# Performance work log

Measured on AMD Instinct MI355X. Metric: run time of the kernel, lower is better.

The kernel has to match this reference:

```python
import jax, jax.numpy as jnp
import numpy as np
from jax import lax


def _viterbi_decode(logits, trans):
    """Batched Viterbi decode (tf.contrib.crf.crf_decode semantics, full lengths).
    logits: [B, T, U] unary potentials; trans: [U, U], trans[i, j] = score(i -> j).
    Returns int32 tags [B, T]."""
    logits_t = jnp.swapaxes(logits, 0, 1)  # [T, B, U]
    init_v = logits_t[0]                   # [B, U]

    def fwd_step(v, logit_t):
        # scores[b, i, j] = v[b, i] + trans[i, j]
        scores = v[:, :, None] + trans[None, :, :]          # [B, U, U]
        bp = jnp.argmax(scores, axis=1).astype(jnp.int32)   # [B, U] best prev tag
        v_new = jnp.max(scores, axis=1) + logit_t           # [B, U]
        return v_new, bp

    v_last, bps = lax.scan(fwd_step, init_v, logits_t[1:])  # bps: [T-1, B, U]
    last_tag = jnp.argmax(v_last, axis=1).astype(jnp.int32)  # [B]

    def bwd_step(tag, bp):
        # tag is the tag at t+1; bp[b, k] = best tag at t given tag k at t+1
        new_tag = jnp.take_along_axis(bp, tag[:, None], axis=1)[:, 0]
        return new_tag, new_tag

    _, tags_prefix = lax.scan(bwd_step, last_tag, bps, reverse=True)  # [T-1, B]
    tags = jnp.concatenate([tags_prefix, last_tag[None, :]], axis=0)  # [T, B]
    return jnp.swapaxes(tags, 0, 1)  # [B, T]


def setup_inputs() -> dict:
    key = jax.random.key(0)
    k0, k1, k2, k3, k4 = jax.random.split(key, 5)
    B, T, D, U = 64, 512, 1024, 128
    x = jax.random.normal(k0, (B, T, D), dtype=jnp.float32)
    kernel = jax.random.normal(k1, (D, U), dtype=jnp.float32) * (1.0 / np.sqrt(D))
    bias = jnp.zeros((U,), dtype=jnp.float32)
    chain_kernel = jax.random.normal(k2, (U, U), dtype=jnp.float32) * 0.1
    left_boundary = jax.random.normal(k3, (U,), dtype=jnp.float32) * 0.1
    right_boundary = jax.random.normal(k4, (U,), dtype=jnp.float32) * 0.1
    return {
        "x": x,
        "kernel": kernel,
        "bias": bias,
        "chain_kernel": chain_kernel,
        "left_boundary": left_boundary,
        "right_boundary": right_boundary,
    }


def reference(x, kernel, bias, chain_kernel, left_boundary, right_boundary):
    # _dense_layer: linear activation, x @ kernel + bias
    logits = jnp.einsum("btd,du->btu", x, kernel) + bias  # [B, T, U]
    # add_boundary_energy with mask=None: boundaries on first / last timestep
    logits = logits.at[:, 0, :].add(left_boundary)
    logits = logits.at[:, -1, :].add(right_boundary)
    # test_mode='viterbi', learn_mode='join': return decoded tags cast to float32
    tags = _viterbi_decode(logits, chain_kernel)
    return tags.astype(jnp.float32)
```

## Files before the change

kernel.cpp:

```cpp
#include <hip/hip_runtime.h>

#define T_SEQ 512
#define U_TAGS 128
#define D_DIM 1024
#define M_ROWS (64 * T_SEQ)

__global__ __launch_bounds__(256, 4) void crf_gemm_part(
    const float* __restrict__ A, const float* __restrict__ Bk,
    float* __restrict__ Cpart, int kdepth) {
  __shared__ float As[16][132];
  __shared__ float Bs[16][132];
  const int tid = threadIdx.x;
  const int tx = tid & 15, ty = tid >> 4;
  const int row0 = blockIdx.x * 128;
  const int kbase = blockIdx.y * kdepth;

  const int am = tid >> 2, ak = (tid & 3) << 2;
  const int bk = tid >> 5, bn = (tid & 31) << 2;

  float acc[8][8] = {};

  float4 a0 = *(const float4*)&A[(size_t)(row0 + am) * D_DIM + kbase + ak];
  float4 a1 = *(const float4*)&A[(size_t)(row0 + am + 64) * D_DIM + kbase + ak];
  float4 b0 = *(const float4*)&Bk[(size_t)(kbase + bk) * U_TAGS + bn];
  float4 b1 = *(const float4*)&Bk[(size_t)(kbase + bk + 8) * U_TAGS + bn];

  for (int k0 = 0; k0 < kdepth; k0 += 16) {
    As[ak + 0][am] = a0.x; As[ak + 1][am] = a0.y;
    As[ak + 2][am] = a0.z; As[ak + 3][am] = a0.w;
    As[ak + 0][am + 64] = a1.x; As[ak + 1][am + 64] = a1.y;
    As[ak + 2][am + 64] = a1.z; As[ak + 3][am + 64] = a1.w;
    *(float4*)&Bs[bk][bn] = b0;
    *(float4*)&Bs[bk + 8][bn] = b1;
    __syncthreads();
    if (k0 + 16 < kdepth) {
      const int kn = kbase + k0 + 16;
      a0 = *(const float4*)&A[(size_t)(row0 + am) * D_DIM + kn + ak];
      a1 = *(const float4*)&A[(size_t)(row0 + am + 64) * D_DIM + kn + ak];
      b0 = *(const float4*)&Bk[(size_t)(kn + bk) * U_TAGS + bn];
      b1 = *(const float4*)&Bk[(size_t)(kn + bk + 8) * U_TAGS + bn];
    }
#pragma unroll
    for (int kk = 0; kk < 16; ++kk) {
      float a[8], b[8];
      *(float4*)&a[0] = *(const float4*)&As[kk][ty * 8];
      *(float4*)&a[4] = *(const float4*)&As[kk][ty * 8 + 4];
      *(float4*)&b[0] = *(const float4*)&Bs[kk][tx * 4];
      *(float4*)&b[4] = *(const float4*)&Bs[kk][tx * 4 + 64];
#pragma unroll
      for (int r = 0; r < 8; ++r)
#pragma unroll
        for (int c = 0; c < 8; ++c) acc[r][c] = fmaf(a[r], b[c], acc[r][c]);
    }
    __syncthreads();
  }

  float* Cp = Cpart + (size_t)blockIdx.y * M_ROWS * U_TAGS;
#pragma unroll
  for (int r = 0; r < 8; ++r) {
    const int row = row0 + ty * 8 + r;
    *(float4*)&Cp[(size_t)row * U_TAGS + tx * 4] = *(float4*)&acc[r][0];
    *(float4*)&Cp[(size_t)row * U_TAGS + tx * 4 + 64] = *(float4*)&acc[r][4];
  }
}

__global__ __launch_bounds__(256) void crf_combine(
    float* __restrict__ p, const float* __restrict__ bias,
    const float* __restrict__ lb, const float* __restrict__ rb, int nparts) {
  const int i = blockIdx.x * 256 + threadIdx.x;
  const int row = i >> 5;
  const int col = (i & 31) << 2;
  const int t = row & (T_SEQ - 1);
  float4 o = *(const float4*)&p[(size_t)i * 4];
  for (int q = 1; q < nparts; ++q) {
    const float* pq = p + (size_t)q * M_ROWS * U_TAGS;
    float4 v = *(const float4*)&pq[(size_t)i * 4];
    o.x += v.x; o.y += v.y; o.z += v.z; o.w += v.w;
  }
  float4 bb = *(const float4*)&bias[col];
  o.x += bb.x; o.y += bb.y; o.z += bb.z; o.w += bb.w;
  if (t == 0) {
    float4 l = *(const float4*)&lb[col];
    o.x += l.x; o.y += l.y; o.z += l.z; o.w += l.w;
  }
  if (t == T_SEQ - 1) {
    float4 r = *(const float4*)&rb[col];
    o.x += r.x; o.y += r.y; o.z += r.z; o.w += r.w;
  }
  *(float4*)&p[(size_t)i * 4] = o;
}

__global__ __launch_bounds__(256) void crf_gemm(
    const float* __restrict__ A, const float* __restrict__ Bk,
    const float* __restrict__ bias, const float* __restrict__ lb,
    const float* __restrict__ rb, float* __restrict__ C) {
  __shared__ float As[16][132];
  __shared__ float Bs[16][132];
  const int tid = threadIdx.x;
  const int tx = tid & 15, ty = tid >> 4;
  const int row0 = blockIdx.x * 128;
  const int am = tid >> 2, ak = (tid & 3) << 2;
  const int bk = tid >> 5, bn = (tid & 31) << 2;
  float acc[8][8] = {};
  float4 a0 = *(const float4*)&A[(size_t)(row0 + am) * D_DIM + ak];
  float4 a1 = *(const float4*)&A[(size_t)(row0 + am + 64) * D_DIM + ak];
  float4 b0 = *(const float4*)&Bk[(size_t)bk * U_TAGS + bn];
  float4 b1 = *(const float4*)&Bk[(size_t)(bk + 8) * U_TAGS + bn];
  for (int k0 = 0; k0 < D_DIM; k0 += 16) {
    As[ak + 0][am] = a0.x; As[ak + 1][am] = a0.y;
    As[ak + 2][am] = a0.z; As[ak + 3][am] = a0.w;
    As[ak + 0][am + 64] = a1.x; As[ak + 1][am + 64] = a1.y;
    As[ak + 2][am + 64] = a1.z; As[ak + 3][am + 64] = a1.w;
    *(float4*)&Bs[bk][bn] = b0;
    *(float4*)&Bs[bk + 8][bn] = b1;
    __syncthreads();
    if (k0 + 16 < D_DIM) {
      a0 = *(const float4*)&A[(size_t)(row0 + am) * D_DIM + k0 + 16 + ak];
      a1 = *(const float4*)&A[(size_t)(row0 + am + 64) * D_DIM + k0 + 16 + ak];
      b0 = *(const float4*)&Bk[(size_t)(k0 + 16 + bk) * U_TAGS + bn];
      b1 = *(const float4*)&Bk[(size_t)(k0 + 16 + bk + 8) * U_TAGS + bn];
    }
#pragma unroll
    for (int kk = 0; kk < 16; ++kk) {
      float a[8], b[8];
      *(float4*)&a[0] = *(const float4*)&As[kk][ty * 8];
      *(float4*)&a[4] = *(const float4*)&As[kk][ty * 8 + 4];
      *(float4*)&b[0] = *(const float4*)&Bs[kk][tx * 4];
      *(float4*)&b[4] = *(const float4*)&Bs[kk][tx * 4 + 64];
#pragma unroll
      for (int r = 0; r < 8; ++r)
#pragma unroll
        for (int c = 0; c < 8; ++c) acc[r][c] = fmaf(a[r], b[c], acc[r][c]);
    }
    __syncthreads();
  }
#pragma unroll
  for (int r = 0; r < 8; ++r) {
    const int row = row0 + ty * 8 + r;
    const int t = row & (T_SEQ - 1);
    const int n0 = tx * 4, n1 = tx * 4 + 64;
    float o[8];
#pragma unroll
    for (int c = 0; c < 4; ++c) {
      float v = acc[r][c] + bias[n0 + c];
      if (t == 0) v += lb[n0 + c];
      if (t == T_SEQ - 1) v += rb[n0 + c];
      o[c] = v;
    }
#pragma unroll
    for (int c = 0; c < 4; ++c) {
      float v = acc[r][c + 4] + bias[n1 + c];
      if (t == 0) v += lb[n1 + c];
      if (t == T_SEQ - 1) v += rb[n1 + c];
      o[c + 4] = v;
    }
    *(float4*)&C[(size_t)row * U_TAGS + n0] = *(float4*)&o[0];
    *(float4*)&C[(size_t)row * U_TAGS + n1] = *(float4*)&o[4];
  }
}

__device__ __forceinline__ float rl_f(float v, int lane) {
  return __int_as_float(__builtin_amdgcn_readlane(__float_as_int(v), lane));
}
template <int CTRL>
__device__ __forceinline__ float dpp_max_step(float x) {
  int v = __float_as_int(x);
  int t = __builtin_amdgcn_update_dpp(v, v, CTRL, 0xF, 0xF, false);
  return fmaxf(x, __int_as_float(t));
}
__device__ __forceinline__ float wave_max64_bcast(float x) {
  x = dpp_max_step<0x111>(x);
  x = dpp_max_step<0x112>(x);
  x = dpp_max_step<0x114>(x);
  x = dpp_max_step<0x118>(x);
  x = dpp_max_step<0x142>(x);
  x = dpp_max_step<0x143>(x);
  return rl_f(x, 63);
}

__global__ __launch_bounds__(256) void crf_viterbi(
    const float* __restrict__ logits,
    const float* __restrict__ trans,
    float* __restrict__ out) {
  __shared__ __align__(16) float trs[U_TAGS * U_TAGS];
  __shared__ __align__(16) unsigned char bp[(T_SEQ - 1) * U_TAGS];
  __shared__ unsigned char tags[T_SEQ];
  __shared__ unsigned char M[8][U_TAGS];
  __shared__ float rmaxs[U_TAGS];
  __shared__ float wmin2[2];
  __shared__ float gminS;
  __shared__ int lastTagS;

  const int b = blockIdx.x;
  const int tid = threadIdx.x;
  const float* lg_b = logits + (size_t)b * T_SEQ * U_TAGS;

#pragma unroll
  for (int it = 0; it < 16; ++it)
    *(float4*)&trs[(it * 256 + tid) * 4] =
        *(const float4*)&trans[(it * 256 + tid) * 4];
  __syncthreads();

  float rowmin = 1e30f;
  if (tid < U_TAGS) {
    float mx = -1e30f, mn = 1e30f;
    for (int q = 0; q < 32; ++q) {
      float4 v = *(const float4*)&trs[tid * U_TAGS + q * 4];
      mx = fmaxf(fmaxf(mx, v.x), fmaxf(v.y, fmaxf(v.z, v.w)));
      mn = fminf(fminf(mn, v.x), fminf(v.y, fminf(v.z, v.w)));
    }
    rmaxs[tid] = mx;
    rowmin = mn;
  }
  if (tid < U_TAGS) {
#pragma unroll
    for (int off = 1; off < 64; off <<= 1)
      rowmin = fminf(rowmin, __shfl_xor(rowmin, off));
    if ((tid & 63) == 0) wmin2[tid >> 6] = rowmin;
  }
  __syncthreads();
  if (tid == 0) gminS = fminf(wmin2[0], wmin2[1]);
  __syncthreads();

  if (tid < 64) {
    const int l = tid;
    float v0 = lg_b[l];
    float v1 = lg_b[64 + l];
    const float gmin = gminS;
    const float c0 = rmaxs[l] - gmin + 0.01f;
    const float c1 = rmaxs[64 + l] - gmin + 0.01f;
    float lgA0 = lg_b[U_TAGS + l], lgA1 = lg_b[U_TAGS + 64 + l];
    float lgB0 = lg_b[2 * U_TAGS + l], lgB1 = lg_b[2 * U_TAGS + 64 + l];

    for (int t = 1; t < T_SEQ; ++t) {
      int tp = t + 2; if (tp > T_SEQ - 1) tp = T_SEQ - 1;
      float lgC0 = lg_b[(size_t)tp * U_TAGS + l];
      float lgC1 = lg_b[(size_t)tp * U_TAGS + 64 + l];

      const float vm = wave_max64_bcast(fmaxf(v0, v1));
      unsigned long long m0 = __ballot(v0 + c0 >= vm);
      unsigned long long m1 = __ballot(v1 + c1 >= vm);

      int a0 = -1, a1 = -1, b0 = -1, b1 = -1;
      if (m0) { a0 = __builtin_ctzll(m0); m0 &= m0 - 1;
        if (m0) { a1 = __builtin_ctzll(m0); m0 &= m0 - 1; } }
      if (m1) { b0 = __builtin_ctzll(m1); m1 &= m1 - 1;
        if (m1) { b1 = __builtin_ctzll(m1); m1 &= m1 - 1; } }

      float tA00 = 0, tA01 = 0, tA10 = 0, tA11 = 0;
      float tB00 = 0, tB01 = 0, tB10 = 0, tB11 = 0;
      if (a0 >= 0) { tA00 = trs[a0 * U_TAGS + l]; tA01 = trs[a0 * U_TAGS + 64 + l]; }
      if (a1 >= 0) { tA10 = trs[a1 * U_TAGS + l]; tA11 = trs[a1 * U_TAGS + 64 + l]; }
      if (b0 >= 0) { tB00 = trs[(64 + b0) * U_TAGS + l]; tB01 = trs[(64 + b0) * U_TAGS + 64 + l]; }
      if (b1 >= 0) { tB10 = trs[(64 + b1) * U_TAGS + l]; tB11 = trs[(64 + b1) * U_TAGS + 64 + l]; }

      float best0 = -1e30f, best1 = -1e30f;
      int bi0 = 0, bi1 = 0;
      if (a0 >= 0) {
        float vi = rl_f(v0, a0);
        float s0 = vi + tA00, s1 = vi + tA01;
        if (s0 > best0) { best0 = s0; bi0 = a0; }
        if (s1 > best1) { best1 = s1; bi1 = a0; }
      }
      if (a1 >= 0) {
        float vi = rl_f(v0, a1);
        float s0 = vi + tA10, s1 = vi + tA11;
        if (s0 > best0) { best0 = s0; bi0 = a1; }
        if (s1 > best1) { best1 = s1; bi1 = a1; }
      }
      while (m0) {
        int i = __builtin_ctzll(m0); m0 &= m0 - 1;
        float vi = rl_f(v0, i);
        float s0 = vi + trs[i * U_TAGS + l], s1 = vi + trs[i * U_TAGS + 64 + l];
        if (s0 > best0) { best0 = s0; bi0 = i; }
        if (s1 > best1) { best1 = s1; bi1 = i; }
      }
      if (b0 >= 0) {
        float vi = rl_f(v1, b0);
        float s0 = vi + tB00, s1 = vi + tB01;
        if (s0 > best0) { best0 = s0; bi0 = 64 + b0; }
        if (s1 > best1) { best1 = s1; bi1 = 64 + b0; }
      }
      if (b1 >= 0) {
        float vi = rl_f(v1, b1);
        float s0 = vi + tB10, s1 = vi + tB11;
        if (s0 > best0) { best0 = s0; bi0 = 64 + b1; }
        if (s1 > best1) { best1 = s1; bi1 = 64 + b1; }
      }
      while (m1) {
        int i = __builtin_ctzll(m1); m1 &= m1 - 1;
        float vi = rl_f(v1, i);
        float s0 = vi + trs[(64 + i) * U_TAGS + l];
        float s1 = vi + trs[(64 + i) * U_TAGS + 64 + l];
        if (s0 > best0) { best0 = s0; bi0 = 64 + i; }
        if (s1 > best1) { best1 = s1; bi1 = 64 + i; }
      }

      bp[(t - 1) * U_TAGS + l] = (unsigned char)bi0;
      bp[(t - 1) * U_TAGS + 64 + l] = (unsigned char)bi1;
      v0 = best0 + lgA0;
      v1 = best1 + lgA1;
      lgA0 = lgB0; lgA1 = lgB1;
      lgB0 = lgC0; lgB1 = lgC1;
    }

    float val = v0; int idx = l;
    if (v1 > v0) { val = v1; idx = 64 + l; }
#pragma unroll
    for (int off = 1; off < 64; off <<= 1) {
      float vo = __shfl_xor(val, off);
      int io = __shfl_xor(idx, off);
      if (vo > val || (vo == val && io < idx)) { val = vo; idx = io; }
    }
    if (l == 0) { lastTagS = idx; tags[T_SEQ - 1] = (unsigned char)idx; }
  }
  __syncthreads();

#pragma unroll
  for (int q = 0; q < 4; ++q) {
    const int chain = tid + q * 256;
    const int c = chain >> 7, s = chain & 127;
    const int lo = c * 64;
    const int hi = (c == 7) ? (T_SEQ - 2) : (c * 64 + 63);
    int cur = s;
    for (int t = hi; t >= lo; --t) cur = bp[t * U_TAGS + cur];
    M[c][s] = (unsigned char)cur;
  }
  __syncthreads();
  __shared__ unsigned char seedE[8];
  if (tid == 0) {
    int e = lastTagS;
    seedE[7] = (unsigned char)e;
    for (int c = 7; c >= 1; --c) { e = M[c][e]; seedE[c - 1] = (unsigned char)e; }
  }
  __syncthreads();
  if (tid < 8) {
    const int c = tid;
    const int lo = c * 64;
    const int hi = (c == 7) ? (T_SEQ - 2) : (c * 64 + 63);
    int cur = seedE[c];
    for (int t = hi; t >= lo; --t) {
      cur = bp[t * U_TAGS + cur];
      tags[t] = (unsigned char)cur;
    }
  }
  __syncthreads();
  out[(size_t)b * T_SEQ + tid] = (float)tags[tid];
  out[(size_t)b * T_SEQ + 256 + tid] = (float)tags[256 + tid];
}

extern "C" void kernel_launch(void* const* d_in, const int* in_sizes, int n_in,
                              void* d_out, int out_size, void* d_ws,
                              size_t ws_size, hipStream_t stream) {
  const float* x = (const float*)d_in[0];
  const float* kern = (const float*)d_in[1];
  const float* bias = (const float*)d_in[2];
  const float* chain = (const float*)d_in[3];
  const float* lb = (const float*)d_in[4];
  const float* rb = (const float*)d_in[5];
  float* out = (float*)d_out;
  float* logits = (float*)d_ws;

  const size_t part = (size_t)M_ROWS * U_TAGS * sizeof(float);
  const int nblk = M_ROWS * U_TAGS / 4 / 256;
  if (ws_size >= 4 * part) {
    crf_gemm_part<<<dim3(256, 4), 256, 0, stream>>>(x, kern, logits, D_DIM / 4);
    crf_combine<<<nblk, 256, 0, stream>>>(logits, bias, lb, rb, 4);
  } else if (ws_size >= 2 * part) {
    crf_gemm_part<<<dim3(256, 2), 256, 0, stream>>>(x, kern, logits, D_DIM / 2);
    crf_combine<<<nblk, 256, 0, stream>>>(logits, bias, lb, rb, 2);
  } else {
    crf_gemm<<<256, 256, 0, stream>>>(x, kern, bias, lb, rb, logits);
  }
  crf_viterbi<<<64, 256, 0, stream>>>(logits, chain, out);
}
```

Baseline: 671.7 us.

## Shrink GEMM tiles to 64 rows and branchlessly unroll Viterbi candidate max

The split-K GEMM now uses 64-row tiles with 128-thread blocks, doubling the block count so more CUs receive work. The Viterbi step handles the first four candidate predecessors per half with branch-free readlanes, LDS loads and a tournament of selects, and falls back to a loop only when more candidates remain. This shortens the serial per-timestep critical path, which dominates since only 64 blocks run. The cost is lower register reuse in the GEMM and extra work when few candidates exist, and tie-breaking between candidates changes.

```diff
diff --git a/kernel.cpp b/kernel.cpp
--- a/kernel.cpp
+++ b/kernel.cpp
@@ -5,40 +5,46 @@
 #define D_DIM 1024
 #define M_ROWS (64 * T_SEQ)
 
-__global__ __launch_bounds__(256, 4) void crf_gemm_part(
+__global__ __launch_bounds__(128) void crf_gemm_part(
     const float* __restrict__ A, const float* __restrict__ Bk,
     float* __restrict__ Cpart, int kdepth) {
-  __shared__ float As[16][132];
+  __shared__ float As[16][68];
   __shared__ float Bs[16][132];
   const int tid = threadIdx.x;
   const int tx = tid & 15, ty = tid >> 4;
-  const int row0 = blockIdx.x * 128;
+  const int row0 = blockIdx.x * 64;
   const int kbase = blockIdx.y * kdepth;
 
-  const int am = tid >> 2, ak = (tid & 3) << 2;
-  const int bk = tid >> 5, bn = (tid & 31) << 2;
+  const int am = tid >> 1, ak = (tid & 1) << 3;
+  const int bk0 = tid >> 5, bn = (tid & 31) << 2;
 
   float acc[8][8] = {};
 
   float4 a0 = *(const float4*)&A[(size_t)(row0 + am) * D_DIM + kbase + ak];
-  float4 a1 = *(const float4*)&A[(size_t)(row0 + am + 64) * D_DIM + kbase + ak];
-  float4 b0 = *(const float4*)&Bk[(size_t)(kbase + bk) * U_TAGS + bn];
-  float4 b1 = *(const float4*)&Bk[(size_t)(kbase + bk + 8) * U_TAGS + bn];
+  float4 a1 = *(const float4*)&A[(size_t)(row0 + am) * D_DIM + kbase + ak + 4];
+  float4 b0 = *(const float4*)&Bk[(size_t)(kbase + bk0) * U_TAGS + bn];
+  float4 b1 = *(const float4*)&Bk[(size_t)(kbase + bk0 + 4) * U_TAGS + bn];
+  float4 b2 = *(const float4*)&Bk[(size_t)(kbase + bk0 + 8) * U_TAGS + bn];
+  float4 b3 = *(const float4*)&Bk[(size_t)(kbase + bk0 + 12) * U_TAGS + bn];
 
   for (int k0 = 0; k0 < kdepth; k0 += 16) {
     As[ak + 0][am] = a0.x; As[ak + 1][am] = a0.y;
     As[ak + 2][am] = a0.z; As[ak + 3][am] = a0.w;
-    As[ak + 0][am + 64] = a1.x; As[ak + 1][am + 64] = a1.y;
-    As[ak + 2][am + 64] = a1.z; As[ak + 3][am + 64] = a1.w;
-    *(float4*)&Bs[bk][bn] = b0;
-    *(float4*)&Bs[bk + 8][bn] = b1;
+    As[ak + 4][am] = a1.x; As[ak + 5][am] = a1.y;
+    As[ak + 6][am] = a1.z; As[ak + 7][am] = a1.w;
+    *(float4*)&Bs[bk0][bn] = b0;
+    *(float4*)&Bs[bk0 + 4][bn] = b1;
+    *(float4*)&Bs[bk0 + 8][bn] = b2;
+    *(float4*)&Bs[bk0 + 12][bn] = b3;
     __syncthreads();
     if (k0 + 16 < kdepth) {
       const int kn = kbase + k0 + 16;
       a0 = *(const float4*)&A[(size_t)(row0 + am) * D_DIM + kn + ak];
-      a1 = *(const float4*)&A[(size_t)(row0 + am + 64) * D_DIM + kn + ak];
-      b0 = *(const float4*)&Bk[(size_t)(kn + bk) * U_TAGS + bn];
-      b1 = *(const float4*)&Bk[(size_t)(kn + bk + 8) * U_TAGS + bn];
+      a1 = *(const float4*)&A[(size_t)(row0 + am) * D_DIM + kn + ak + 4];
+      b0 = *(const float4*)&Bk[(size_t)(kn + bk0) * U_TAGS + bn];
+      b1 = *(const float4*)&Bk[(size_t)(kn + bk0 + 4) * U_TAGS + bn];
+      b2 = *(const float4*)&Bk[(size_t)(kn + bk0 + 8) * U_TAGS + bn];
+      b3 = *(const float4*)&Bk[(size_t)(kn + bk0 + 12) * U_TAGS + bn];
     }
 #pragma unroll
     for (int kk = 0; kk < 16; ++kk) {
@@ -177,6 +183,12 @@
   x = dpp_max_step<0x143>(x);
   return rl_f(x, 63);
 }
+__device__ __forceinline__ void win(float sa, int ia, float sb, int ib,
+                                    float& so, int& io) {
+  bool g = sa >= sb;
+  so = g ? sa : sb;
+  io = g ? ia : ib;
+}
 
 __global__ __launch_bounds__(256) void crf_viterbi(
     const float* __restrict__ logits,
@@ -241,65 +253,78 @@
       unsigned long long m0 = __ballot(v0 + c0 >= vm);
       unsigned long long m1 = __ballot(v1 + c1 >= vm);
 
-      int a0 = -1, a1 = -1, b0 = -1, b1 = -1;
-      if (m0) { a0 = __builtin_ctzll(m0); m0 &= m0 - 1;
-        if (m0) { a1 = __builtin_ctzll(m0); m0 &= m0 - 1; } }
-      if (m1) { b0 = __builtin_ctzll(m1); m1 &= m1 - 1;
-        if (m1) { b1 = __builtin_ctzll(m1); m1 &= m1 - 1; } }
-
-      float tA00 = 0, tA01 = 0, tA10 = 0, tA11 = 0;
-      float tB00 = 0, tB01 = 0, tB10 = 0, tB11 = 0;
-      if (a0 >= 0) { tA00 = trs[a0 * U_TAGS + l]; tA01 = trs[a0 * U_TAGS + 64 + l]; }
-      if (a1 >= 0) { tA10 = trs[a1 * U_TAGS + l]; tA11 = trs[a1 * U_TAGS + 64 + l]; }
-      if (b0 >= 0) { tB00 = trs[(64 + b0) * U_TAGS + l]; tB01 = trs[(64 + b0) * U_TAGS + 64 + l]; }
-      if (b1 >= 0) { tB10 = trs[(64 + b1) * U_TAGS + l]; tB11 = trs[(64 + b1) * U_TAGS + 64 + l]; }
-
-      float best0 = -1e30f, best1 = -1e30f;
-      int bi0 = 0, bi1 = 0;
-      if (a0 >= 0) {
-        float vi = rl_f(v0, a0);
-        float s0 = vi + tA00, s1 = vi + tA01;
-        if (s0 > best0) { best0 = s0; bi0 = a0; }
-        if (s1 > best1) { best1 = s1; bi1 = a0; }
+      unsigned long long r0 = m0, r1 = m1;
+      int i0[4], i1[4];
+      bool f0[4], f1[4];
+#pragma unroll
+      for (int s = 0; s < 4; ++s) {
+        f0[s] = (r0 != 0ull);
+        i0[s] = __builtin_ctzll(r0 | 0x8000000000000000ull);
+        r0 &= r0 - 1;
+        f1[s] = (r1 != 0ull);
+        i1[s] = __builtin_ctzll(r1 | 0x8000000000000000ull);
+        r1 &= r1 - 1;
       }
-      if (a1 >= 0) {
-        float vi = rl_f(v0, a1);
-        float s0 = vi + tA10, s1 = vi + tA11;
-        if (s0 > best0) { best0 = s0; bi0 = a1; }
-        if (s1 > best1) { best1 = s1; bi1 = a1; }
+      float sv0[4], sv1[4];
+#pragma unroll
+      for (int s = 0; s < 4; ++s) {
+        sv0[s] = f0[s] ? rl_f(v0, i0[s]) : -1e30f;
+        sv1[s] = f1[s] ? rl_f(v1, i1[s]) : -1e30f;
       }
-      while (m0) {
-        int i = __builtin_ctzll(m0); m0 &= m0 - 1;
-        float vi = rl_f(v0, i);
-        float s0 = vi + trs[i * U_TAGS + l], s1 = vi + trs[i * U_TAGS + 64 + l];
-        if (s0 > best0) { best0 = s0; bi0 = i; }
-        if (s1 > best1) { best1 = s1; bi1 = i; }
+      float tA[4][2], tB[4][2];
+#pragma unroll
+      for (int s = 0; s < 4; ++s) {
+        const float* pA = &trs[i0[s] * U_TAGS + l];
+        tA[s][0] = pA[0]; tA[s][1] = pA[64];
+        const float* pB = &trs[(64 + i1[s]) * U_TAGS + l];
+        tB[s][0] = pB[0]; tB[s][1] = pB[64];
       }
-      if (b0 >= 0) {
-        float vi = rl_f(v1, b0);
-        float s0 = vi + tB00, s1 = vi + tB01;
-        if (s0 > best0) { best0 = s0; bi0 = 64 + b0; }
-        if (s1 > best1) { best1 = s1; bi1 = 64 + b0; }
+      float sAL[4], sAH[4], sBL[4], sBH[4];
+#pragma unroll
+      for (int s = 0; s < 4; ++s) {
+        sAL[s] = sv0[s] + tA[s][0]; sAH[s] = sv0[s] + tA[s][1];
+        sBL[s] = sv1[s] + tB[s][0]; sBH[s] = sv1[s] + tB[s][1];
       }
-      if (b1 >= 0) {
-        float vi = rl_f(v1, b1);
-        float s0 = vi + tB10, s1 = vi + tB11;
-        if (s0 > best0) { best0 = s0; bi0 = 64 + b1; }
-        if (s1 > best1) { best1 = s1; bi1 = 64 + b1; }
+      float wL, wL2, wL3, wL4, wH, wH2, wH3, wH4;
+      int xL, xL2, xL3, xL4, xH, xH2, xH3, xH4;
+      win(sAL[0], i0[0], sAL[1], i0[1], wL, xL);
+      win(sAL[2], i0[2], sAL[3], i0[3], wL2, xL2);
+      win(sBL[0], 64 + i1[0], sBL[1], 64 + i1[1], wL3, xL3);
+      win(sBL[2], 64 + i1[2], sBL[3], 64 + i1[3], wL4, xL4);
+      win(wL, xL, wL2, xL2, wL, xL);
+      win(wL3, xL3, wL4, xL4, wL3, xL3);
+      win(wL, xL, wL3, xL3, wL, xL);
+      win(sAH[0], i0[0], sAH[1], i0[1], wH, xH);
+      win(sAH[2], i0[2], sAH[3], i0[3], wH2, xH2);
+      win(sBH[0], 64 + i1[0], sBH[1], 64 + i1[1], wH3, xH3);
+      win(sBH[2], 64 + i1[2], sBH[3], 64 + i1[3], wH4, xH4);
+      win(wH, xH, wH2, xH2, wH, xH);
+      win(wH3, xH3, wH4, xH4, wH3, xH3);
+      win(wH, xH, wH3, xH3, wH, xH);
+
+      if (r0 | r1) {
+        while (r0) {
+          int i = __builtin_ctzll(r0); r0 &= r0 - 1;
+          float vi = rl_f(v0, i);
+          float sL = vi + trs[i * U_TAGS + l];
+          float sH = vi + trs[i * U_TAGS + 64 + l];
+          if (sL > wL || (sL == wL && i < xL)) { wL = sL; xL = i; }
+          if (sH > wH || (sH == wH && i < xH)) { wH = sH; xH = i; }
+        }
+        while (r1) {
+          int i = __builtin_ctzll(r1); r1 &= r1 - 1;
+          float vi = rl_f(v1, i);
+          float sL = vi + trs[(64 + i) * U_TAGS + l];
+          float sH = vi + trs[(64 + i) * U_TAGS + 64 + l];
+          if (sL > wL || (sL == wL && 64 + i < xL)) { wL = sL; xL = 64 + i; }
+          if (sH > wH || (sH == wH && 64 + i < xH)) { wH = sH; xH = 64 + i; }
+        }
       }
-      while (m1) {
-        int i = __builtin_ctzll(m1); m1 &= m1 - 1;
-        float vi = rl_f(v1, i);
-        float s0 = vi + trs[(64 + i) * U_TAGS + l];
-        float s1 = vi + trs[(64 + i) * U_TAGS + 64 + l];
-        if (s0 > best0) { best0 = s0; bi0 = 64 + i; }
-        if (s1 > best1) { best1 = s1; bi1 = 64 + i; }
-      }
-
-      bp[(t - 1) * U_TAGS + l] = (unsigned char)bi0;
-      bp[(t - 1) * U_TAGS + 64 + l] = (unsigned char)bi1;
-      v0 = best0 + lgA0;
-      v1 = best1 + lgA1;
+
+      bp[(t - 1) * U_TAGS + l] = (unsigned char)xL;
+      bp[(t - 1) * U_TAGS + 64 + l] = (unsigned char)xH;
+      v0 = wL + lgA0;
+      v1 = wH + lgA1;
       lgA0 = lgB0; lgA1 = lgB1;
       lgB0 = lgC0; lgB1 = lgC1;
     }
@@ -364,10 +389,10 @@
   const size_t part = (size_t)M_ROWS * U_TAGS * sizeof(float);
   const int nblk = M_ROWS * U_TAGS / 4 / 256;
   if (ws_size >= 4 * part) {
-    crf_gemm_part<<<dim3(256, 4), 256, 0, stream>>>(x, kern, logits, D_DIM / 4);
+    crf_gemm_part<<<dim3(512, 4), 128, 0, stream>>>(x, kern, logits, D_DIM / 4);
     crf_combine<<<nblk, 256, 0, stream>>>(logits, bias, lb, rb, 4);
   } else if (ws_size >= 2 * part) {
-    crf_gemm_part<<<dim3(256, 2), 256, 0, stream>>>(x, kern, logits, D_DIM / 2);
+    crf_gemm_part<<<dim3(512, 2), 128, 0, stream>>>(x, kern, logits, D_DIM / 2);
     crf_combine<<<nblk, 256, 0, stream>>>(logits, bias, lb, rb, 2);
   } else {
     crf_gemm<<<256, 256, 0, stream>>>(x, kern, bias, lb, rb, logits);
```

Result: no change. 668.0 us (-0.5%).

## Add producer-wave logit prefetch ring and branchless top-3 Viterbi selection; use 2-way split-K

Applied to the files above, without the earlier changes.

The Viterbi kernel now dedicates a second wavefront to streaming each sequence's logits from global memory into a 4-slot shared-memory ring buffer, synchronised through volatile flags. The compute wave reads each step's logits from LDS instead of issuing global loads inside the serial recurrence. The candidate-predecessor search is also rebuilt as an unconditional top-3-per-half selection with select-based comparisons, falling back to a loop only when there are more candidates. Separately, the GEMM drops the 4-way split-K path for a fixed 2-way split, which halves the combine kernel's partial-sum reads but lowers GEMM grid parallelism. The spin-wait handshake between waves risks stalls and relies on LDS memory ordering.

```diff
diff --git a/kernel.cpp b/kernel.cpp
--- a/kernel.cpp
+++ b/kernel.cpp
@@ -5,15 +5,15 @@
 #define D_DIM 1024
 #define M_ROWS (64 * T_SEQ)
 
-__global__ __launch_bounds__(256, 4) void crf_gemm_part(
+__global__ __launch_bounds__(256) void crf_gemm_half(
     const float* __restrict__ A, const float* __restrict__ Bk,
-    float* __restrict__ Cpart, int kdepth) {
+    float* __restrict__ Cpart) {
   __shared__ float As[16][132];
   __shared__ float Bs[16][132];
   const int tid = threadIdx.x;
   const int tx = tid & 15, ty = tid >> 4;
   const int row0 = blockIdx.x * 128;
-  const int kbase = blockIdx.y * kdepth;
+  const int kbase = blockIdx.y * (D_DIM / 2);
 
   const int am = tid >> 2, ak = (tid & 3) << 2;
   const int bk = tid >> 5, bn = (tid & 31) << 2;
@@ -25,7 +25,7 @@
   float4 b0 = *(const float4*)&Bk[(size_t)(kbase + bk) * U_TAGS + bn];
   float4 b1 = *(const float4*)&Bk[(size_t)(kbase + bk + 8) * U_TAGS + bn];
 
-  for (int k0 = 0; k0 < kdepth; k0 += 16) {
+  for (int k0 = 0; k0 < D_DIM / 2; k0 += 16) {
     As[ak + 0][am] = a0.x; As[ak + 1][am] = a0.y;
     As[ak + 2][am] = a0.z; As[ak + 3][am] = a0.w;
     As[ak + 0][am + 64] = a1.x; As[ak + 1][am + 64] = a1.y;
@@ -33,7 +33,7 @@
     *(float4*)&Bs[bk][bn] = b0;
     *(float4*)&Bs[bk + 8][bn] = b1;
     __syncthreads();
-    if (k0 + 16 < kdepth) {
+    if (k0 + 16 < D_DIM / 2) {
       const int kn = kbase + k0 + 16;
       a0 = *(const float4*)&A[(size_t)(row0 + am) * D_DIM + kn + ak];
       a1 = *(const float4*)&A[(size_t)(row0 + am + 64) * D_DIM + kn + ak];
@@ -66,19 +66,18 @@
 
 __global__ __launch_bounds__(256) void crf_combine(
     float* __restrict__ p, const float* __restrict__ bias,
-    const float* __restrict__ lb, const float* __restrict__ rb, int nparts) {
+    const float* __restrict__ lb, const float* __restrict__ rb) {
   const int i = blockIdx.x * 256 + threadIdx.x;
   const int row = i >> 5;
   const int col = (i & 31) << 2;
   const int t = row & (T_SEQ - 1);
-  float4 o = *(const float4*)&p[(size_t)i * 4];
-  for (int q = 1; q < nparts; ++q) {
-    const float* pq = p + (size_t)q * M_ROWS * U_TAGS;
-    float4 v = *(const float4*)&pq[(size_t)i * 4];
-    o.x += v.x; o.y += v.y; o.z += v.z; o.w += v.w;
-  }
+  const float* p1 = p + (size_t)M_ROWS * U_TAGS;
+  float4 v0 = *(const float4*)&p[(size_t)i * 4];
+  float4 v1 = *(const float4*)&p1[(size_t)i * 4];
   float4 bb = *(const float4*)&bias[col];
-  o.x += bb.x; o.y += bb.y; o.z += bb.z; o.w += bb.w;
+  float4 o;
+  o.x = v0.x + v1.x + bb.x; o.y = v0.y + v1.y + bb.y;
+  o.z = v0.z + v1.z + bb.z; o.w = v0.w + v1.w + bb.w;
   if (t == 0) {
     float4 l = *(const float4*)&lb[col];
     o.x += l.x; o.y += l.y; o.z += l.z; o.w += l.w;
@@ -177,6 +176,12 @@
   x = dpp_max_step<0x143>(x);
   return rl_f(x, 63);
 }
+__device__ __forceinline__ void win(float sa, int ia, float sb, int ib,
+                                    float& so, int& io) {
+  bool g = sa >= sb;
+  so = g ? sa : sb;
+  io = g ? ia : ib;
+}
 
 __global__ __launch_bounds__(256) void crf_viterbi(
     const float* __restrict__ logits,
@@ -184,8 +189,11 @@
     float* __restrict__ out) {
   __shared__ __align__(16) float trs[U_TAGS * U_TAGS];
   __shared__ __align__(16) unsigned char bp[(T_SEQ - 1) * U_TAGS];
+  __shared__ __align__(16) float ring[4 * 8 * U_TAGS];
+  __shared__ int flags[2];
   __shared__ unsigned char tags[T_SEQ];
   __shared__ unsigned char M[8][U_TAGS];
+  __shared__ unsigned char seedE[8];
   __shared__ float rmaxs[U_TAGS];
   __shared__ float wmin2[2];
   __shared__ float gminS;
@@ -199,6 +207,7 @@
   for (int it = 0; it < 16; ++it)
     *(float4*)&trs[(it * 256 + tid) * 4] =
         *(const float4*)&trans[(it * 256 + tid) * 4];
+  if (tid == 0) { flags[0] = 0; flags[1] = 0; }
   __syncthreads();
 
   float rowmin = 1e30f;
@@ -211,8 +220,6 @@
     }
     rmaxs[tid] = mx;
     rowmin = mn;
-  }
-  if (tid < U_TAGS) {
 #pragma unroll
     for (int off = 1; off < 64; off <<= 1)
       rowmin = fminf(rowmin, __shfl_xor(rowmin, off));
@@ -222,86 +229,111 @@
   if (tid == 0) gminS = fminf(wmin2[0], wmin2[1]);
   __syncthreads();
 
-  if (tid < 64) {
-    const int l = tid;
-    float v0 = lg_b[l];
-    float v1 = lg_b[64 + l];
-    const float gmin = gminS;
-    const float c0 = rmaxs[l] - gmin + 0.01f;
-    const float c1 = rmaxs[64 + l] - gmin + 0.01f;
-    float lgA0 = lg_b[U_TAGS + l], lgA1 = lg_b[U_TAGS + 64 + l];
-    float lgB0 = lg_b[2 * U_TAGS + l], lgB1 = lg_b[2 * U_TAGS + 64 + l];
+  const int wv = tid >> 6, l = tid & 63;
+  volatile int* vfl = (volatile int*)flags;
+
+  if (wv == 1) {
+    const float4* src = (const float4*)lg_b;
+    float4* dst = (float4*)ring;
+    for (int c = 0; c < 64; ++c) {
+      while (vfl[1] + 4 <= c) { }
+      const float4* s4 = src + c * 256;
+      float4 d0 = s4[l], d1 = s4[l + 64], d2 = s4[l + 128], d3 = s4[l + 192];
+      float4* d4 = dst + (c & 3) * 256;
+      d4[l] = d0; d4[l + 64] = d1; d4[l + 128] = d2; d4[l + 192] = d3;
+      __threadfence_block();
+      if (l == 0) vfl[0] = c + 1;
+    }
+  } else if (wv == 0) {
+    const float cc0 = rmaxs[l] - gminS + 0.01f;
+    const float cc1 = rmaxs[64 + l] - gminS + 0.01f;
+    while (vfl[0] < 1) { }
+    float v0 = ring[l];
+    float v1 = ring[64 + l];
+    const unsigned long long G = 0x8000000000000000ull;
+    int bpoff = l;
 
     for (int t = 1; t < T_SEQ; ++t) {
-      int tp = t + 2; if (tp > T_SEQ - 1) tp = T_SEQ - 1;
-      float lgC0 = lg_b[(size_t)tp * U_TAGS + l];
-      float lgC1 = lg_b[(size_t)tp * U_TAGS + 64 + l];
+      if ((t & 7) == 0) {
+        const int c = t >> 3;
+        if (l == 0) vfl[1] = c;
+        while (vfl[0] <= c) { }
+      }
+      const float* sl = ring + ((t >> 3) & 3) * 1024 + (t & 7) * U_TAGS;
+      float lg0 = sl[l];
+      float lg1 = sl[64 + l];
 
       const float vm = wave_max64_bcast(fmaxf(v0, v1));
-      unsigned long long m0 = __ballot(v0 + c0 >= vm);
-      unsigned long long m1 = __ballot(v1 + c1 >= vm);
-
-      int a0 = -1, a1 = -1, b0 = -1, b1 = -1;
-      if (m0) { a0 = __builtin_ctzll(m0); m0 &= m0 - 1;
-        if (m0) { a1 = __builtin_ctzll(m0); m0 &= m0 - 1; } }
-      if (m1) { b0 = __builtin_ctzll(m1); m1 &= m1 - 1;
-        if (m1) { b1 = __builtin_ctzll(m1); m1 &= m1 - 1; } }
-
-      float tA00 = 0, tA01 = 0, tA10 = 0, tA11 = 0;
-      float tB00 = 0, tB01 = 0, tB10 = 0, tB11 = 0;
-      if (a0 >= 0) { tA00 = trs[a0 * U_TAGS + l]; tA01 = trs[a0 * U_TAGS + 64 + l]; }
-      if (a1 >= 0) { tA10 = trs[a1 * U_TAGS + l]; tA11 = trs[a1 * U_TAGS + 64 + l]; }
-      if (b0 >= 0) { tB00 = trs[(64 + b0) * U_TAGS + l]; tB01 = trs[(64 + b0) * U_TAGS + 64 + l]; }
-      if (b1 >= 0) { tB10 = trs[(64 + b1) * U_TAGS + l]; tB11 = trs[(64 + b1) * U_TAGS + 64 + l]; }
-
-      float best0 = -1e30f, best1 = -1e30f;
-      int bi0 = 0, bi1 = 0;
-      if (a0 >= 0) {
-        float vi = rl_f(v0, a0);
-        float s0 = vi + tA00, s1 = vi + tA01;
-        if (s0 > best0) { best0 = s0; bi0 = a0; }
-        if (s1 > best1) { best1 = s1; bi1 = a0; }
+      unsigned long long m0 = __ballot(v0 + cc0 >= vm);
+      unsigned long long m1 = __ballot(v1 + cc1 >= vm);
+
+      unsigned long long rA1 = m0 & (m0 - 1), rA2 = rA1 & (rA1 - 1);
+      unsigned long long rB1 = m1 & (m1 - 1), rB2 = rB1 & (rB1 - 1);
+      const int iA0 = __builtin_ctzll(m0 | G);
+      const int iA1 = __builtin_ctzll(rA1 | G);
+      const int iA2 = __builtin_ctzll(rA2 | G);
+      const int iB0 = __builtin_ctzll(m1 | G);
+      const int iB1 = __builtin_ctzll(rB1 | G);
+      const int iB2 = __builtin_ctzll(rB2 | G);
+      unsigned long long tail = (rA2 & (rA2 - 1)) | (rB2 & (rB2 - 1));
+
+      const float svA0 = rl_f(v0, iA0), svA1 = rl_f(v0, iA1),
+                  svA2 = rl_f(v0, iA2);
+      const float svB0 = rl_f(v1, iB0), svB1 = rl_f(v1, iB1),
+                  svB2 = rl_f(v1, iB2);
+
+      const float* pA0 = &trs[iA0 * U_TAGS + l];
+      const float* pA1 = &trs[iA1 * U_TAGS + l];
+      const float* pA2 = &trs[iA2 * U_TAGS + l];
+      const float* pB0 = &trs[(64 + iB0) * U_TAGS + l];
+      const float* pB1 = &trs[(64 + iB1) * U_TAGS + l];
+      const float* pB2 = &trs[(64 + iB2) * U_TAGS + l];
+      const float tA0L = pA0[0], tA0H = pA0[64];
+      const float tA1L = pA1[0], tA1H = pA1[64];
+      const float tA2L = pA2[0], tA2H = pA2[64];
+      const float tB0L = pB0[0], tB0H = pB0[64];
+      const float tB1L = pB1[0], tB1H = pB1[64];
+      const float tB2L = pB2[0], tB2H = pB2[64];
+
+      float wa, wb, wL; int xa, xb, xL;
+      win(svA0 + tA0L, iA0, svA1 + tA1L, iA1, wa, xa);
+      win(wa, xa, svA2 + tA2L, iA2, wa, xa);
+      win(svB0 + tB0L, 64 + iB0, svB1 + tB1L, 64 + iB1, wb, xb);
+      win(wb, xb, svB2 + tB2L, 64 + iB2, wb, xb);
+      win(wa, xa, wb, xb, wL, xL);
+      float wH; int xH;
+      win(svA0 + tA0H, iA0, svA1 + tA1H, iA1, wa, xa);
+      win(wa, xa, svA2 + tA2H, iA2, wa, xa);
+      win(svB0 + tB0H, 64 + iB0, svB1 + tB1H, 64 + iB1, wb, xb);
+      win(wb, xb, svB2 + tB2H, 64 + iB2, wb, xb);
+      win(wa, xa, wb, xb, wH, xH);
+
+      if (tail) {
+        unsigned long long r = rA2 & (rA2 - 1);
+        while (r) {
+          int i = __builtin_ctzll(r); r &= r - 1;
+          float vi = rl_f(v0, i);
+          float sL = vi + trs[i * U_TAGS + l];
+          float sH = vi + trs[i * U_TAGS + 64 + l];
+          if (sL > wL || (sL == wL && i < xL)) { wL = sL; xL = i; }
+          if (sH > wH || (sH == wH && i < xH)) { wH = sH; xH = i; }
+        }
+        r = rB2 & (rB2 - 1);
+        while (r) {
+          int i = __builtin_ctzll(r); r &= r - 1;
+          float vi = rl_f(v1, i);
+          float sL = vi + trs[(64 + i) * U_TAGS + l];
+          float sH = vi + trs[(64 + i) * U_TAGS + 64 + l];
+          if (sL > wL || (sL == wL && 64 + i < xL)) { wL = sL; xL = 64 + i; }
+          if (sH > wH || (sH == wH && 64 + i < xH)) { wH = sH; xH = 64 + i; }
+        }
       }
-      if (a1 >= 0) {
-        float vi = rl_f(v0, a1);
-        float s0 = vi + tA10, s1 = vi + tA11;
-        if (s0 > best0) { best0 = s0; bi0 = a1; }
-        if (s1 > best1) { best1 = s1; bi1 = a1; }
-      }
-      while (m0) {
-        int i = __builtin_ctzll(m0); m0 &= m0 - 1;
-        float vi = rl_f(v0, i);
-        float s0 = vi + trs[i * U_TAGS + l], s1 = vi + trs[i * U_TAGS + 64 + l];
-        if (s0 > best0) { best0 = s0; bi0 = i; }
-        if (s1 > best1) { best1 = s1; bi1 = i; }
-      }
-      if (b0 >= 0) {
-        float vi = rl_f(v1, b0);
-        float s0 = vi + tB00, s1 = vi + tB01;
-        if (s0 > best0) { best0 = s0; bi0 = 64 + b0; }
-        if (s1 > best1) { best1 = s1; bi1 = 64 + b0; }
-      }
-      if (b1 >= 0) {
-        float vi = rl_f(v1, b1);
-        float s0 = vi + tB10, s1 = vi + tB11;
-        if (s0 > best0) { best0 = s0; bi0 = 64 + b1; }
-        if (s1 > best1) { best1 = s1; bi1 = 64 + b1; }
-      }
-      while (m1) {
-        int i = __builtin_ctzll(m1); m1 &= m1 - 1;
-        float vi = rl_f(v1, i);
-        float s0 = vi + trs[(64 + i) * U_TAGS + l];
-        float s1 = vi + trs[(64 + i) * U_TAGS + 64 + l];
-        if (s0 > best0) { best0 = s0; bi0 = 64 + i; }
-        if (s1 > best1) { best1 = s1; bi1 = 64 + i; }
-      }
-
-      bp[(t - 1) * U_TAGS + l] = (unsigned char)bi0;
-      bp[(t - 1) * U_TAGS + 64 + l] = (unsigned char)bi1;
-      v0 = best0 + lgA0;
-      v1 = best1 + lgA1;
-      lgA0 = lgB0; lgA1 = lgB1;
-      lgB0 = lgC0; lgB1 = lgC1;
+
+      bp[bpoff] = (unsigned char)xL;
+      bp[bpoff + 64] = (unsigned char)xH;
+      bpoff += U_TAGS;
+      v0 = wL + lg0;
+      v1 = wH + lg1;
     }
 
     float val = v0; int idx = l;
@@ -327,7 +359,6 @@
     M[c][s] = (unsigned char)cur;
   }
   __syncthreads();
-  __shared__ unsigned char seedE[8];
   if (tid == 0) {
     int e = lastTagS;
     seedE[7] = (unsigned char)e;
@@ -362,13 +393,10 @@
   float* logits = (float*)d_ws;
 
   const size_t part = (size_t)M_ROWS * U_TAGS * sizeof(float);
-  const int nblk = M_ROWS * U_TAGS / 4 / 256;
-  if (ws_size >= 4 * part) {
-    crf_gemm_part<<<dim3(256, 4), 256, 0, stream>>>(x, kern, logits, D_DIM / 4);
-    crf_combine<<<nblk, 256, 0, stream>>>(logits, bias, lb, rb, 4);
-  } else if (ws_size >= 2 * part) {
-    crf_gemm_part<<<dim3(256, 2), 256, 0, stream>>>(x, kern, logits, D_DIM / 2);
-    crf_combine<<<nblk, 256, 0, stream>>>(logits, bias, lb, rb, 2);
+  if (ws_size >= 2 * part) {
+    crf_gemm_half<<<dim3(256, 2), 256, 0, stream>>>(x, kern, logits);
+    crf_combine<<<(M_ROWS * U_TAGS / 4 + 255) / 256, 256, 0, stream>>>(
+        logits, bias, lb, rb);
   } else {
     crf_gemm<<<256, 256, 0, stream>>>(x, kern, bias, lb, rb, logits);
   }
```

Result: faster. 589.7 us (-12.2%).
